# Kernel optimization log

Hardware: AMD Instinct MI355X
Metric: run time of the kernel (lower is better)

## Reference

```python
import jax, jax.numpy as jnp
import numpy as np

C = 16          # total channels = 3 image + 12 hidden + 1 output
NIMG = 3        # immutable image channels
HID = 128
FIRE_RATE = 0.5
SOBEL_X = np.outer([1, 2, 1], [-1, 0, 1]) / 8.0
SOBEL_Y = SOBEL_X.T


def _depthwise3x3(x, filt):
    # x: [B,H,W,C] channels-last; same 3x3 filter applied per channel (groups=C)
    k = jnp.asarray(filt, jnp.float32).reshape(3, 3, 1, 1) * jnp.ones((1, 1, 1, C), jnp.float32)
    return jax.lax.conv_general_dilated(
        x, k, window_strides=(1, 1), padding='SAME',
        dimension_numbers=('NHWC', 'HWIO', 'NHWC'), feature_group_count=C)


def setup_inputs() -> dict:
    key = jax.random.key(0)
    k1, k2, k3, k4 = jax.random.split(key, 4)
    B, H, W = 16, 256, 256
    x = jax.random.normal(k1, (B, H, W, C), jnp.float32)
    # NB: original zero-inits w_out (trivial dx=0); use small random weights so the
    w_hidden = jax.random.normal(k2, (C * 3, HID), jnp.float32) * 0.05
    b_hidden = jnp.zeros((HID,), jnp.float32)
    w_out = jax.random.normal(k3, (HID, C), jnp.float32) * 0.05
    rand_u = jax.random.uniform(k4, (B, H, W, 1), jnp.float32)  # stochastic fire mask source
    return {'x': x, 'w_hidden': w_hidden, 'b_hidden': b_hidden,
            'w_out': w_out, 'rand_u': rand_u, 'steps': 1}


def reference(x, w_hidden, b_hidden, w_out, rand_u, steps):
    # immutable image channels: dx[..., :NIMG] = 0
    immut = jnp.concatenate([jnp.zeros((NIMG,), x.dtype), jnp.ones((C - NIMG,), x.dtype)])
    fire = (rand_u > FIRE_RATE).astype(x.dtype)  # [B,H,W,1]
    for _ in range(steps):
        # perceive: [x, sobel_x(x), sobel_y(x)] -> [B,H,W,3C]
        y = jnp.concatenate([x, _depthwise3x3(x, SOBEL_X), _depthwise3x3(x, SOBEL_Y)], axis=-1)
        # per-cell 2-layer MLP
        h = jax.nn.relu(jnp.einsum('bhwf,fk->bhwk', y, w_hidden) + b_hidden)
        dx = jnp.einsum('bhwk,kc->bhwc', h, w_out)
        # stochastic fire-rate mask + immutable image channels, residual add
        x = x + dx * fire * immut
        # use_alive_mask=False -> life mask is identically 1 (no-op)
    return x
```

## Files before the change

kernel.cpp:

```cpp
#include <hip/hip_runtime.h>

#define NCH 16
#define HID 128

typedef __attribute__((ext_vector_type(8))) short s16x8;
typedef __attribute__((ext_vector_type(4))) float f32x4;

__device__ __forceinline__ unsigned short f2bf(float f) {
    __bf16 b = (__bf16)f;
    return __builtin_bit_cast(unsigned short, b);
}
__device__ __forceinline__ unsigned pk2(float a, float b) {
    return (unsigned)f2bf(a) | ((unsigned)f2bf(b) << 16);
}

__global__ __launch_bounds__(256, 3) void nca_mfma(
    const float* __restrict__ x,
    const float* __restrict__ wh,
    const float* __restrict__ bh,
    const float* __restrict__ wo,
    const float* __restrict__ ru,
    float* __restrict__ out)
{
    __shared__ __align__(16) char smem[25920 + 18432 + 512];
    float* s_xf = (float*)smem;
    unsigned short (*s_wht)[72]    = (unsigned short(*)[72])(smem + 25920);
    unsigned short (*s_h)[16][136] = (unsigned short(*)[16][136])(smem + 25920);
    float* s_bh = (float*)(smem + 25920 + 18432);

    const int tid = threadIdx.x;
    const int w = tid >> 6, lane = tid & 63;
    const int p = lane & 15, g = lane >> 4;

    const int sb   = (blockIdx.x & 7) * 512 + (blockIdx.x >> 3);
    const int img  = sb >> 8, rem = sb & 255;
    const int ti16 = (rem >> 4) << 4;
    const int tj16 = (rem & 15) << 4;
    const int ibase = img << 16;

    const float4* x4 = (const float4*)x;
    float4* o4 = (float4*)out;

    {
        const int R0 = ti16 - 1, C0 = tj16 - 1;
        for (int idx = tid; idx < 18 * 18 * 4; idx += 256) {
            const int q = idx & 3, pp = idx >> 2;
            const int r = pp / 18, c = pp - r * 18;
            const int ir = R0 + r, jc = C0 + c;
            float4 v = make_float4(0.f, 0.f, 0.f, 0.f);
            if (((unsigned)ir < 256u) & ((unsigned)jc < 256u))
                v = x4[(ibase + (ir << 8) + jc) * 4 + q];
            *(float4*)&s_xf[pp * 20 + 4 * q] = v;
        }
    }

    float ruv[4];
    #pragma unroll
    for (int k = 0; k < 4; ++k)
        ruv[k] = ru[ibase + ((ti16 + 4 * w + k) << 8) + tj16 + p];

    for (int idx = tid; idx < 48 * HID; idx += 256) {
        int f = idx >> 7, n = idx & 127;
        int part = f >> 4, c = f & 15;
        int gg = c >> 2, i2 = c & 3;
        int k = (part == 0) ? (8 * gg + i2)
              : (part == 1) ? (8 * gg + 4 + i2)
                            : (32 + 8 * gg + i2);
        s_wht[n][k] = f2bf(wh[idx]);
    }
    for (int idx = tid; idx < HID * 16; idx += 256) {
        int n = idx >> 4, q = idx & 15;
        s_wht[n][36 + 8 * (q >> 2) + (q & 3)] = 0;
    }
    if (tid < HID) s_bh[tid] = bh[tid];
    __syncthreads();

    s16x8 whf[2][8];
    #pragma unroll
    for (int t = 0; t < 8; ++t)
        #pragma unroll
        for (int s = 0; s < 2; ++s)
            whf[s][t] = *(const s16x8*)&s_wht[p + 16 * t][s * 32 + 8 * g];

    s16x8 wof[4];
    #pragma unroll
    for (int kk = 0; kk < 4; ++kk) {
        s16x8 v;
        #pragma unroll
        for (int i2 = 0; i2 < 8; ++i2)
            v[i2] = (short)f2bf(wo[(kk * 32 + 8 * g + i2) * NCH + p]);
        wof[kk] = v;
    }
    __syncthreads();

    const float m0 = (g == 0) ? 0.f : 1.f;

    #pragma unroll 2
    for (int k = 0; k < 4; ++k) {
        const int tr = 4 * w + k;
        const int pix = ibase + ((ti16 + tr) << 8) + tj16 + p;

        const float* tp = &s_xf[(tr * 18 + p) * 20 + 4 * g];
        const f32x4 t00 = *(const f32x4*)(tp + 0);
        const f32x4 t01 = *(const f32x4*)(tp + 20);
        const f32x4 t02 = *(const f32x4*)(tp + 40);
        const f32x4 t10 = *(const f32x4*)(tp + 360);
        const f32x4 t11 = *(const f32x4*)(tp + 380);
        const f32x4 t12 = *(const f32x4*)(tp + 400);
        const f32x4 t20 = *(const f32x4*)(tp + 720);
        const f32x4 t21 = *(const f32x4*)(tp + 740);
        const f32x4 t22 = *(const f32x4*)(tp + 760);

        f32x4 sxv, syv;
        #pragma unroll
        for (int e = 0; e < 4; ++e) {
            sxv[e] = 0.125f * ((t02[e] - t00[e]) + (t22[e] - t20[e]))
                   + 0.25f  * (t12[e] - t10[e]);
            syv[e] = 0.125f * ((t20[e] - t00[e]) + (t22[e] - t02[e]))
                   + 0.25f  * (t21[e] - t01[e]);
        }

        s16x8 bf0, bf1;
        {
            unsigned w0 = pk2(t11[0], t11[1]), w1 = pk2(t11[2], t11[3]);
            unsigned w2 = pk2(sxv[0], sxv[1]), w3 = pk2(sxv[2], sxv[3]);
            unsigned w4 = pk2(syv[0], syv[1]), w5 = pk2(syv[2], syv[3]);
            bf0[0] = (short)(w0 & 0xffff); bf0[1] = (short)(w0 >> 16);
            bf0[2] = (short)(w1 & 0xffff); bf0[3] = (short)(w1 >> 16);
            bf0[4] = (short)(w2 & 0xffff); bf0[5] = (short)(w2 >> 16);
            bf0[6] = (short)(w3 & 0xffff); bf0[7] = (short)(w3 >> 16);
            bf1[0] = (short)(w4 & 0xffff); bf1[1] = (short)(w4 >> 16);
            bf1[2] = (short)(w5 & 0xffff); bf1[3] = (short)(w5 >> 16);
            bf1[4] = 0; bf1[5] = 0; bf1[6] = 0; bf1[7] = 0;
        }

        f32x4 acc[8];
        #pragma unroll
        for (int t = 0; t < 8; ++t)
            acc[t] = *(const f32x4*)&s_bh[16 * t + 4 * g];
        #pragma unroll
        for (int t = 0; t < 8; ++t)
            acc[t] = __builtin_amdgcn_mfma_f32_16x16x32_bf16(whf[0][t], bf0, acc[t], 0, 0, 0);
        #pragma unroll
        for (int t = 0; t < 8; ++t)
            acc[t] = __builtin_amdgcn_mfma_f32_16x16x32_bf16(whf[1][t], bf1, acc[t], 0, 0, 0);

        #pragma unroll
        for (int t = 0; t < 8; ++t) {
            uint2 hw;
            hw.x = pk2(fmaxf(acc[t][0], 0.f), fmaxf(acc[t][1], 0.f));
            hw.y = pk2(fmaxf(acc[t][2], 0.f), fmaxf(acc[t][3], 0.f));
            *(uint2*)&s_h[w][p][16 * t + 4 * g] = hw;
        }

        f32x4 acc2 = {0.f, 0.f, 0.f, 0.f};
        #pragma unroll
        for (int kk = 0; kk < 4; ++kk) {
            s16x8 hf = *(const s16x8*)&s_h[w][p][kk * 32 + 8 * g];
            acc2 = __builtin_amdgcn_mfma_f32_16x16x32_bf16(wof[kk], hf, acc2, 0, 0, 0);
        }

        const float fire = (ruv[k] > 0.5f) ? 1.f : 0.f;
        float4 o;
        o.x = t11[0] + acc2[0] * fire * m0;
        o.y = t11[1] + acc2[1] * fire * m0;
        o.z = t11[2] + acc2[2] * fire * m0;
        o.w = t11[3] + acc2[3] * fire;
        o4[pix * 4 + g] = o;
    }
}

extern "C" void kernel_launch(void* const* d_in, const int* in_sizes, int n_in,
                              void* d_out, int out_size, void* d_ws, size_t ws_size,
                              hipStream_t stream) {
    const float* x  = (const float*)d_in[0];
    const float* wh = (const float*)d_in[1];
    const float* bh = (const float*)d_in[2];
    const float* wo = (const float*)d_in[3];
    const float* ru = (const float*)d_in[4];
    float* out = (float*)d_out;

    nca_mfma<<<4096, 256, 0, stream>>>(x, wh, bh, wo, ru, out);
}
```

Baseline: 174.0 us.

## Pre-convert weights to bf16 in a prep kernel and load fragments from global

Adds a small prep kernel that converts the hidden and output weights to bf16, already in MFMA fragment layout, inside a workspace buffer. The main kernel then loads its weight fragments straight from global memory instead of converting and staging them in LDS for every block, which drops one barrier and the per-block conversion work. Dropping the weight staging shrinks LDS, so the main kernel's launch bound goes from 3 to 4 blocks per SM. The halo tile row stride is also reduced from 20 to 16 floats, which may add LDS bank conflicts, and the extra kernel launch adds fixed overhead.

```diff
diff --git a/kernel.cpp b/kernel.cpp
--- a/kernel.cpp
+++ b/kernel.cpp
@@ -14,19 +14,42 @@
     return (unsigned)f2bf(a) | ((unsigned)f2bf(b) << 16);
 }
 
-__global__ __launch_bounds__(256, 3) void nca_mfma(
+
+__global__ void prep_weights(const float* __restrict__ wh,
+                             const float* __restrict__ wo,
+                             unsigned short* __restrict__ ws) {
+    const int idx = blockIdx.x * 256 + threadIdx.x;
+    if (idx < 6144) {
+        const int f = idx >> 7, n = idx & 127;
+        const int part = f >> 4, c = f & 15;
+        const int gg = c >> 2, i2 = c & 3;
+        const int k = (part == 0) ? (8 * gg + i2)
+                    : (part == 1) ? (8 * gg + 4 + i2)
+                                  : (32 + 8 * gg + i2);
+        ws[n * 64 + k] = f2bf(wh[idx]);
+    } else if (idx < 8192) {
+        const int r = idx - 6144;
+        const int n = r >> 4, q = r & 15;
+        ws[n * 64 + 36 + 8 * (q >> 2) + (q & 3)] = 0;
+    } else if (idx < 10240) {
+        const int r = idx - 8192;
+        const int i2 = r & 7, rem = r >> 3;
+        const int p = rem & 15, gk = rem >> 4;
+        const int g = gk & 3, kk = gk >> 2;
+        ws[8192 + r] = f2bf(wo[(kk * 32 + 8 * g + i2) * NCH + p]);
+    }
+}
+
+__global__ __launch_bounds__(256, 4) void nca_mfma(
     const float* __restrict__ x,
-    const float* __restrict__ wh,
     const float* __restrict__ bh,
-    const float* __restrict__ wo,
     const float* __restrict__ ru,
-    float* __restrict__ out)
+    float* __restrict__ out,
+    const unsigned short* __restrict__ wsw)
 {
-    __shared__ __align__(16) char smem[25920 + 18432 + 512];
-    float* s_xf = (float*)smem;
-    unsigned short (*s_wht)[72]    = (unsigned short(*)[72])(smem + 25920);
-    unsigned short (*s_h)[16][136] = (unsigned short(*)[16][136])(smem + 25920);
-    float* s_bh = (float*)(smem + 25920 + 18432);
+    __shared__ __align__(16) float s_xf[324 * 16];
+    __shared__ __align__(16) unsigned short s_h[4][16][136];
+    __shared__ __align__(16) float s_bh[HID];
 
     const int tid = threadIdx.x;
     const int w = tid >> 6, lane = tid & 63;
@@ -50,47 +73,28 @@
             float4 v = make_float4(0.f, 0.f, 0.f, 0.f);
             if (((unsigned)ir < 256u) & ((unsigned)jc < 256u))
                 v = x4[(ibase + (ir << 8) + jc) * 4 + q];
-            *(float4*)&s_xf[pp * 20 + 4 * q] = v;
+            *(float4*)&s_xf[pp * 16 + 4 * q] = v;
         }
     }
+    if (tid < HID) s_bh[tid] = bh[tid];
 
     float ruv[4];
     #pragma unroll
     for (int k = 0; k < 4; ++k)
         ruv[k] = ru[ibase + ((ti16 + 4 * w + k) << 8) + tj16 + p];
 
-    for (int idx = tid; idx < 48 * HID; idx += 256) {
-        int f = idx >> 7, n = idx & 127;
-        int part = f >> 4, c = f & 15;
-        int gg = c >> 2, i2 = c & 3;
-        int k = (part == 0) ? (8 * gg + i2)
-              : (part == 1) ? (8 * gg + 4 + i2)
-                            : (32 + 8 * gg + i2);
-        s_wht[n][k] = f2bf(wh[idx]);
-    }
-    for (int idx = tid; idx < HID * 16; idx += 256) {
-        int n = idx >> 4, q = idx & 15;
-        s_wht[n][36 + 8 * (q >> 2) + (q & 3)] = 0;
-    }
-    if (tid < HID) s_bh[tid] = bh[tid];
-    __syncthreads();
-
     s16x8 whf[2][8];
     #pragma unroll
     for (int t = 0; t < 8; ++t)
         #pragma unroll
         for (int s = 0; s < 2; ++s)
-            whf[s][t] = *(const s16x8*)&s_wht[p + 16 * t][s * 32 + 8 * g];
+            whf[s][t] = *(const s16x8*)&wsw[(p + 16 * t) * 64 + s * 32 + 8 * g];
 
     s16x8 wof[4];
     #pragma unroll
-    for (int kk = 0; kk < 4; ++kk) {
-        s16x8 v;
-        #pragma unroll
-        for (int i2 = 0; i2 < 8; ++i2)
-            v[i2] = (short)f2bf(wo[(kk * 32 + 8 * g + i2) * NCH + p]);
-        wof[kk] = v;
-    }
+    for (int kk = 0; kk < 4; ++kk)
+        wof[kk] = *(const s16x8*)&wsw[8192 + ((kk * 4 + g) * 16 + p) * 8];
+
     __syncthreads();
 
     const float m0 = (g == 0) ? 0.f : 1.f;
@@ -100,16 +104,16 @@
         const int tr = 4 * w + k;
         const int pix = ibase + ((ti16 + tr) << 8) + tj16 + p;
 
-        const float* tp = &s_xf[(tr * 18 + p) * 20 + 4 * g];
+        const float* tp = &s_xf[(tr * 18 + p) * 16 + 4 * g];
         const f32x4 t00 = *(const f32x4*)(tp + 0);
-        const f32x4 t01 = *(const f32x4*)(tp + 20);
-        const f32x4 t02 = *(const f32x4*)(tp + 40);
-        const f32x4 t10 = *(const f32x4*)(tp + 360);
-        const f32x4 t11 = *(const f32x4*)(tp + 380);
-        const f32x4 t12 = *(const f32x4*)(tp + 400);
-        const f32x4 t20 = *(const f32x4*)(tp + 720);
-        const f32x4 t21 = *(const f32x4*)(tp + 740);
-        const f32x4 t22 = *(const f32x4*)(tp + 760);
+        const f32x4 t01 = *(const f32x4*)(tp + 16);
+        const f32x4 t02 = *(const f32x4*)(tp + 32);
+        const f32x4 t10 = *(const f32x4*)(tp + 288);
+        const f32x4 t11 = *(const f32x4*)(tp + 304);
+        const f32x4 t12 = *(const f32x4*)(tp + 320);
+        const f32x4 t20 = *(const f32x4*)(tp + 576);
+        const f32x4 t21 = *(const f32x4*)(tp + 592);
+        const f32x4 t22 = *(const f32x4*)(tp + 608);
 
         f32x4 sxv, syv;
         #pragma unroll
@@ -120,19 +124,11 @@
                    + 0.25f  * (t21[e] - t01[e]);
         }
 
-        s16x8 bf0, bf1;
-        {
-            unsigned w0 = pk2(t11[0], t11[1]), w1 = pk2(t11[2], t11[3]);
-            unsigned w2 = pk2(sxv[0], sxv[1]), w3 = pk2(sxv[2], sxv[3]);
-            unsigned w4 = pk2(syv[0], syv[1]), w5 = pk2(syv[2], syv[3]);
-            bf0[0] = (short)(w0 & 0xffff); bf0[1] = (short)(w0 >> 16);
-            bf0[2] = (short)(w1 & 0xffff); bf0[3] = (short)(w1 >> 16);
-            bf0[4] = (short)(w2 & 0xffff); bf0[5] = (short)(w2 >> 16);
-            bf0[6] = (short)(w3 & 0xffff); bf0[7] = (short)(w3 >> 16);
-            bf1[0] = (short)(w4 & 0xffff); bf1[1] = (short)(w4 >> 16);
-            bf1[2] = (short)(w5 & 0xffff); bf1[3] = (short)(w5 >> 16);
-            bf1[4] = 0; bf1[5] = 0; bf1[6] = 0; bf1[7] = 0;
-        }
+        const unsigned w0 = pk2(t11[0], t11[1]), w1 = pk2(t11[2], t11[3]);
+        const unsigned w2 = pk2(sxv[0], sxv[1]), w3 = pk2(sxv[2], sxv[3]);
+        const unsigned w4 = pk2(syv[0], syv[1]), w5 = pk2(syv[2], syv[3]);
+        const s16x8 bf0 = __builtin_bit_cast(s16x8, make_uint4(w0, w1, w2, w3));
+        const s16x8 bf1 = __builtin_bit_cast(s16x8, make_uint4(w4, w5, 0u, 0u));
 
         f32x4 acc[8];
         #pragma unroll
@@ -179,6 +175,8 @@
     const float* wo = (const float*)d_in[3];
     const float* ru = (const float*)d_in[4];
     float* out = (float*)d_out;
+    unsigned short* ws = (unsigned short*)d_ws;
 
-    nca_mfma<<<4096, 256, 0, stream>>>(x, wh, bh, wo, ru, out);
+    prep_weights<<<40, 256, 0, stream>>>(wh, wo, ws);
+    nca_mfma<<<4096, 256, 0, stream>>>(x, bh, ru, out, ws);
 }
```

Result: slower. 421.6 us (+142.3%).

## Process four 16x16 tiles per block to amortize weight staging

Applied to the files above, without the earlier changes.

Each block now handles a 16x64 strip, looping over four 16x16 tiles and re-staging the halo between phases, so the MLP weight conversion and fragment loads are done once per four tiles instead of once per tile. The grid shrinks from 4096 to 1024 blocks. Halo padding is reduced from 20 to 16 floats per pixel, which lowers LDS use so launch bounds can ask for 4 blocks per CU. The cost is two extra barriers per phase, halo loads that are not overlapped with compute, and possible LDS bank conflicts from the unpadded stride.

```diff
diff --git a/kernel.cpp b/kernel.cpp
--- a/kernel.cpp
+++ b/kernel.cpp
@@ -14,7 +14,7 @@
     return (unsigned)f2bf(a) | ((unsigned)f2bf(b) << 16);
 }
 
-__global__ __launch_bounds__(256, 3) void nca_mfma(
+__global__ __launch_bounds__(256, 4) void nca_mfma(
     const float* __restrict__ x,
     const float* __restrict__ wh,
     const float* __restrict__ bh,
@@ -22,43 +22,46 @@
     const float* __restrict__ ru,
     float* __restrict__ out)
 {
-    __shared__ __align__(16) char smem[25920 + 18432 + 512];
+    __shared__ __align__(16) char smem[20736 + 18432 + 512];
     float* s_xf = (float*)smem;
-    unsigned short (*s_wht)[72]    = (unsigned short(*)[72])(smem + 25920);
-    unsigned short (*s_h)[16][136] = (unsigned short(*)[16][136])(smem + 25920);
-    float* s_bh = (float*)(smem + 25920 + 18432);
+    unsigned short (*s_wht)[72]    = (unsigned short(*)[72])(smem + 20736);
+    unsigned short (*s_h)[16][136] = (unsigned short(*)[16][136])(smem + 20736);
+    float* s_bh = (float*)(smem + 20736 + 18432);
 
     const int tid = threadIdx.x;
     const int w = tid >> 6, lane = tid & 63;
     const int p = lane & 15, g = lane >> 4;
 
-    const int sb   = (blockIdx.x & 7) * 512 + (blockIdx.x >> 3);
-    const int img  = sb >> 8, rem = sb & 255;
-    const int ti16 = (rem >> 4) << 4;
-    const int tj16 = (rem & 15) << 4;
+    const int sb   = (blockIdx.x & 7) * 128 + (blockIdx.x >> 3);
+    const int img  = sb >> 6, rem = sb & 63;
+    const int ti16 = (rem >> 2) << 4;
+    const int tj64 = (rem & 3) << 6;
     const int ibase = img << 16;
 
     const float4* x4 = (const float4*)x;
     float4* o4 = (float4*)out;
 
-    {
-        const int R0 = ti16 - 1, C0 = tj16 - 1;
-        for (int idx = tid; idx < 18 * 18 * 4; idx += 256) {
-            const int q = idx & 3, pp = idx >> 2;
-            const int r = pp / 18, c = pp - r * 18;
-            const int ir = R0 + r, jc = C0 + c;
-            float4 v = make_float4(0.f, 0.f, 0.f, 0.f);
-            if (((unsigned)ir < 256u) & ((unsigned)jc < 256u))
-                v = x4[(ibase + (ir << 8) + jc) * 4 + q];
-            *(float4*)&s_xf[pp * 20 + 4 * q] = v;
+    auto stage_halo = [&](int C0) {
+        const int R0 = ti16 - 1;
+        #pragma unroll
+        for (int s2 = 0; s2 < 2; ++s2) {
+            const int pp = tid + 256 * s2;
+            if (pp < 324) {
+                const int r = pp / 18, c = pp - r * 18;
+                const int ir = R0 + r, jc = C0 + c;
+                const bool v = ((unsigned)ir < 256u) & ((unsigned)jc < 256u);
+                const float4* src = &x4[(v ? (ibase + (ir << 8) + jc) : ibase) * 4];
+                float4* dst = (float4*)&s_xf[pp * 16];
+                #pragma unroll
+                for (int q = 0; q < 4; ++q) {
+                    float4 t = src[q];
+                    dst[q] = v ? t : make_float4(0.f, 0.f, 0.f, 0.f);
+                }
+            }
         }
-    }
+    };
 
-    float ruv[4];
-    #pragma unroll
-    for (int k = 0; k < 4; ++k)
-        ruv[k] = ru[ibase + ((ti16 + 4 * w + k) << 8) + tj16 + p];
-
+    stage_halo(tj64 - 1);
     for (int idx = tid; idx < 48 * HID; idx += 256) {
         int f = idx >> 7, n = idx & 127;
         int part = f >> 4, c = f & 15;
@@ -95,78 +98,86 @@
 
     const float m0 = (g == 0) ? 0.f : 1.f;
 
-    #pragma unroll 2
-    for (int k = 0; k < 4; ++k) {
-        const int tr = 4 * w + k;
-        const int pix = ibase + ((ti16 + tr) << 8) + tj16 + p;
+    #pragma unroll 1
+    for (int ph = 0; ph < 4; ++ph) {
+        const int tj16 = tj64 + 16 * ph;
 
-        const float* tp = &s_xf[(tr * 18 + p) * 20 + 4 * g];
-        const f32x4 t00 = *(const f32x4*)(tp + 0);
-        const f32x4 t01 = *(const f32x4*)(tp + 20);
-        const f32x4 t02 = *(const f32x4*)(tp + 40);
-        const f32x4 t10 = *(const f32x4*)(tp + 360);
-        const f32x4 t11 = *(const f32x4*)(tp + 380);
-        const f32x4 t12 = *(const f32x4*)(tp + 400);
-        const f32x4 t20 = *(const f32x4*)(tp + 720);
-        const f32x4 t21 = *(const f32x4*)(tp + 740);
-        const f32x4 t22 = *(const f32x4*)(tp + 760);
+        float ruv[4];
+        #pragma unroll
+        for (int k = 0; k < 4; ++k)
+            ruv[k] = ru[ibase + ((ti16 + 4 * w + k) << 8) + tj16 + p];
 
-        f32x4 sxv, syv;
-        #pragma unroll
-        for (int e = 0; e < 4; ++e) {
-            sxv[e] = 0.125f * ((t02[e] - t00[e]) + (t22[e] - t20[e]))
-                   + 0.25f  * (t12[e] - t10[e]);
-            syv[e] = 0.125f * ((t20[e] - t00[e]) + (t22[e] - t02[e]))
-                   + 0.25f  * (t21[e] - t01[e]);
+        #pragma unroll 2
+        for (int k = 0; k < 4; ++k) {
+            const int tr = 4 * w + k;
+            const int pix = ibase + ((ti16 + tr) << 8) + tj16 + p;
+
+            const float* tp = &s_xf[(tr * 18 + p) * 16 + 4 * g];
+            const f32x4 t00 = *(const f32x4*)(tp + 0);
+            const f32x4 t01 = *(const f32x4*)(tp + 16);
+            const f32x4 t02 = *(const f32x4*)(tp + 32);
+            const f32x4 t10 = *(const f32x4*)(tp + 288);
+            const f32x4 t11 = *(const f32x4*)(tp + 304);
+            const f32x4 t12 = *(const f32x4*)(tp + 320);
+            const f32x4 t20 = *(const f32x4*)(tp + 576);
+            const f32x4 t21 = *(const f32x4*)(tp + 592);
+            const f32x4 t22 = *(const f32x4*)(tp + 608);
+
+            f32x4 sxv, syv;
+            #pragma unroll
+            for (int e = 0; e < 4; ++e) {
+                sxv[e] = 0.125f * ((t02[e] - t00[e]) + (t22[e] - t20[e]))
+                       + 0.25f  * (t12[e] - t10[e]);
+                syv[e] = 0.125f * ((t20[e] - t00[e]) + (t22[e] - t02[e]))
+                       + 0.25f  * (t21[e] - t01[e]);
+            }
+
+            const unsigned w0 = pk2(t11[0], t11[1]), w1 = pk2(t11[2], t11[3]);
+            const unsigned w2 = pk2(sxv[0], sxv[1]), w3 = pk2(sxv[2], sxv[3]);
+            const unsigned w4 = pk2(syv[0], syv[1]), w5 = pk2(syv[2], syv[3]);
+            const s16x8 bf0 = __builtin_bit_cast(s16x8, make_uint4(w0, w1, w2, w3));
+            const s16x8 bf1 = __builtin_bit_cast(s16x8, make_uint4(w4, w5, 0u, 0u));
+
+            f32x4 acc[8];
+            #pragma unroll
+            for (int t = 0; t < 8; ++t)
+                acc[t] = *(const f32x4*)&s_bh[16 * t + 4 * g];
+            #pragma unroll
+            for (int t = 0; t < 8; ++t)
+                acc[t] = __builtin_amdgcn_mfma_f32_16x16x32_bf16(whf[0][t], bf0, acc[t], 0, 0, 0);
+            #pragma unroll
+            for (int t = 0; t < 8; ++t)
+                acc[t] = __builtin_amdgcn_mfma_f32_16x16x32_bf16(whf[1][t], bf1, acc[t], 0, 0, 0);
+
+            #pragma unroll
+            for (int t = 0; t < 8; ++t) {
+                uint2 hw;
+                hw.x = pk2(fmaxf(acc[t][0], 0.f), fmaxf(acc[t][1], 0.f));
+                hw.y = pk2(fmaxf(acc[t][2], 0.f), fmaxf(acc[t][3], 0.f));
+                *(uint2*)&s_h[w][p][16 * t + 4 * g] = hw;
+            }
+
+            f32x4 acc2 = {0.f, 0.f, 0.f, 0.f};
+            #pragma unroll
+            for (int kk = 0; kk < 4; ++kk) {
+                s16x8 hf = *(const s16x8*)&s_h[w][p][kk * 32 + 8 * g];
+                acc2 = __builtin_amdgcn_mfma_f32_16x16x32_bf16(wof[kk], hf, acc2, 0, 0, 0);
+            }
+
+            const float fire = (ruv[k] > 0.5f) ? 1.f : 0.f;
+            float4 o;
+            o.x = t11[0] + acc2[0] * fire * m0;
+            o.y = t11[1] + acc2[1] * fire * m0;
+            o.z = t11[2] + acc2[2] * fire * m0;
+            o.w = t11[3] + acc2[3] * fire;
+            o4[pix * 4 + g] = o;
         }
 
-        s16x8 bf0, bf1;
-        {
-            unsigned w0 = pk2(t11[0], t11[1]), w1 = pk2(t11[2], t11[3]);
-            unsigned w2 = pk2(sxv[0], sxv[1]), w3 = pk2(sxv[2], sxv[3]);
-            unsigned w4 = pk2(syv[0], syv[1]), w5 = pk2(syv[2], syv[3]);
-            bf0[0] = (short)(w0 & 0xffff); bf0[1] = (short)(w0 >> 16);
-            bf0[2] = (short)(w1 & 0xffff); bf0[3] = (short)(w1 >> 16);
-            bf0[4] = (short)(w2 & 0xffff); bf0[5] = (short)(w2 >> 16);
-            bf0[6] = (short)(w3 & 0xffff); bf0[7] = (short)(w3 >> 16);
-            bf1[0] = (short)(w4 & 0xffff); bf1[1] = (short)(w4 >> 16);
-            bf1[2] = (short)(w5 & 0xffff); bf1[3] = (short)(w5 >> 16);
-            bf1[4] = 0; bf1[5] = 0; bf1[6] = 0; bf1[7] = 0;
+        if (ph < 3) {
+            __syncthreads();
+            stage_halo(tj64 + 16 * (ph + 1) - 1);
+            __syncthreads();
         }
-
-        f32x4 acc[8];
-        #pragma unroll
-        for (int t = 0; t < 8; ++t)
-            acc[t] = *(const f32x4*)&s_bh[16 * t + 4 * g];
-        #pragma unroll
-        for (int t = 0; t < 8; ++t)
-            acc[t] = __builtin_amdgcn_mfma_f32_16x16x32_bf16(whf[0][t], bf0, acc[t], 0, 0, 0);
-        #pragma unroll
-        for (int t = 0; t < 8; ++t)
-            acc[t] = __builtin_amdgcn_mfma_f32_16x16x32_bf16(whf[1][t], bf1, acc[t], 0, 0, 0);
-
-        #pragma unroll
-        for (int t = 0; t < 8; ++t) {
-            uint2 hw;
-            hw.x = pk2(fmaxf(acc[t][0], 0.f), fmaxf(acc[t][1], 0.f));
-            hw.y = pk2(fmaxf(acc[t][2], 0.f), fmaxf(acc[t][3], 0.f));
-            *(uint2*)&s_h[w][p][16 * t + 4 * g] = hw;
-        }
-
-        f32x4 acc2 = {0.f, 0.f, 0.f, 0.f};
-        #pragma unroll
-        for (int kk = 0; kk < 4; ++kk) {
-            s16x8 hf = *(const s16x8*)&s_h[w][p][kk * 32 + 8 * g];
-            acc2 = __builtin_amdgcn_mfma_f32_16x16x32_bf16(wof[kk], hf, acc2, 0, 0, 0);
-        }
-
-        const float fire = (ruv[k] > 0.5f) ? 1.f : 0.f;
-        float4 o;
-        o.x = t11[0] + acc2[0] * fire * m0;
-        o.y = t11[1] + acc2[1] * fire * m0;
-        o.z = t11[2] + acc2[2] * fire * m0;
-        o.w = t11[3] + acc2[3] * fire;
-        o4[pix * 4 + g] = o;
     }
 }
 
@@ -180,5 +191,5 @@
     const float* ru = (const float*)d_in[4];
     float* out = (float*)d_out;
 
-    nca_mfma<<<4096, 256, 0, stream>>>(x, wh, bh, wo, ru, out);
+    nca_mfma<<<1024, 256, 0, stream>>>(x, wh, bh, wo, ru, out);
 }
```

Result: slower. 280.9 us (+61.5%).
